# Kernel optimization log

Measured on AMD Instinct MI355X. Metric: run time of the kernel, lower is better.

## Reference

```python
import jax, jax.numpy as jnp
import numpy as np

D_MODEL = 1024
HEADS = 16
D_K = D_MODEL // HEADS


def setup_inputs() -> dict:
    key = jax.random.key(0)
    ks = jax.random.split(key, 9)
    s = 1.0 / np.sqrt(D_MODEL)
    x = jax.random.normal(ks[0], (4, 2048, D_MODEL), dtype=jnp.float32)
    Wq = jax.random.uniform(ks[1], (D_MODEL, D_MODEL), jnp.float32, -s, s)
    Wk = jax.random.uniform(ks[2], (D_MODEL, D_MODEL), jnp.float32, -s, s)
    Wv = jax.random.uniform(ks[3], (D_MODEL, D_MODEL), jnp.float32, -s, s)
    Wo = jax.random.uniform(ks[4], (D_MODEL, D_MODEL), jnp.float32, -s, s)
    bq = jax.random.uniform(ks[5], (D_MODEL,), jnp.float32, -s, s)
    bk = jax.random.uniform(ks[6], (D_MODEL,), jnp.float32, -s, s)
    bv = jax.random.uniform(ks[7], (D_MODEL,), jnp.float32, -s, s)
    bo = jax.random.uniform(ks[8], (D_MODEL,), jnp.float32, -s, s)
    return {"x": x, "Wq": Wq, "bq": bq, "Wk": Wk, "bk": bk,
            "Wv": Wv, "bv": bv, "Wo": Wo, "bo": bo}


def reference(x, Wq, bq, Wk, bk, Wv, bv, Wo, bo):
    B, T, C = x.shape
    H, d_k = HEADS, D_K
    # QKV projections (weights stored as [in, out] -> x @ W + b)
    q = (x @ Wq + bq).reshape(B, T, H, d_k).transpose(0, 2, 1, 3)  # [B,H,T,d_k]
    k = (x @ Wk + bk).reshape(B, T, H, d_k).transpose(0, 2, 1, 3)
    v = (x @ Wv + bv).reshape(B, T, H, d_k).transpose(0, 2, 1, 3)
    scores = jnp.einsum('bhqd,bhkd->bhqk', q, k) / jnp.sqrt(jnp.float32(d_k))
    attn = jax.nn.softmax(scores, axis=-1)
    out = jnp.einsum('bhqk,bhkd->bhqd', attn, v)  # [B,H,T,d_k]
    out = out.transpose(0, 2, 1, 3).reshape(B, T, C)
    return out @ Wo + bo
```

## Files before the change

kernel.cpp:

```cpp
#include <hip/hip_runtime.h>
#include <stdint.h>

typedef _Float16 f16;
typedef _Float16 f16x8 __attribute__((ext_vector_type(8)));
typedef float    f32x4 __attribute__((ext_vector_type(4)));
typedef unsigned int u32x4 __attribute__((ext_vector_type(4)));
typedef unsigned int u32x2 __attribute__((ext_vector_type(2)));
typedef unsigned short u16;

#define MFMA16(A,B,C) __builtin_amdgcn_mfma_f32_16x16x32_f16(A,B,C,0,0,0)

__device__ __forceinline__ void gload_lds16(const void* g, void* l) {
  auto gp = reinterpret_cast<const __attribute__((address_space(1))) unsigned int*>(
      reinterpret_cast<uintptr_t>(g));
  auto lp = reinterpret_cast<__attribute__((address_space(3))) unsigned int*>(
      reinterpret_cast<uintptr_t>(l));
  __builtin_amdgcn_global_load_lds(gp, lp, 16, 0, 0);
}

__device__ __forceinline__ unsigned pk16(float a, float b) {
  unsigned short ua = __builtin_bit_cast(unsigned short, (f16)a);
  unsigned short ub = __builtin_bit_cast(unsigned short, (f16)b);
  return ((unsigned)ub << 16) | (unsigned)ua;
}
__device__ __forceinline__ unsigned pk2rtz(float a, float b) {
  return __builtin_bit_cast(unsigned, __builtin_amdgcn_cvt_pkrtz(a, b));
}
__device__ __forceinline__ float ex2(float x) {
  float r; asm("v_exp_f32 %0, %1" : "=v"(r) : "v"(x)); return r;
}
__device__ __forceinline__ f16x8 asf16(u32x4 v) { return __builtin_bit_cast(f16x8, v); }

#define LOG2E 1.44269504088896f

__global__ __launch_bounds__(256) void k_cvt(const float* __restrict__ in,
                                             u16* __restrict__ out, int n8) {
  int i = blockIdx.x * 256 + threadIdx.x;
  if (i >= n8) return;
  const float4* p = (const float4*)in + (size_t)i * 2;
  float4 a = p[0], b = p[1];
  u32x4 o = { pk16(a.x, a.y), pk16(a.z, a.w), pk16(b.x, b.y), pk16(b.z, b.w) };
  *((u32x4*)out + i) = o;
}

__global__ __launch_bounds__(256) void k_transw(const float* __restrict__ Wq, const float* __restrict__ Wk,
                                                const float* __restrict__ Wv, const float* __restrict__ Wo,
                                                u16* __restrict__ WTq, u16* __restrict__ WTk,
                                                u16* __restrict__ WTv, u16* __restrict__ WTo) {
  int z = blockIdx.z;
  const float* W = (z == 0) ? Wq : (z == 1) ? Wk : (z == 2) ? Wv : Wo;
  u16* WT = (z == 0) ? WTq : (z == 1) ? WTk : (z == 2) ? WTv : WTo;
  __shared__ float tile[64][65];
  int tid = threadIdx.x;
  int r0 = blockIdx.y * 64, c0 = blockIdx.x * 64;
#pragma unroll
  for (int i = 0; i < 4; ++i) {
    int idx = tid + i * 256;
    int row = idx >> 4, ch = (idx & 15) * 4;
    float4 v = *(const float4*)&W[(size_t)(r0 + row) * 1024 + c0 + ch];
    tile[row][ch + 0] = v.x; tile[row][ch + 1] = v.y;
    tile[row][ch + 2] = v.z; tile[row][ch + 3] = v.w;
  }
  __syncthreads();
#pragma unroll
  for (int i = 0; i < 4; ++i) {
    int idx = tid + i * 256;
    int orow = idx >> 4, ch = (idx & 15) * 4;
    u32x2 o = { pk16(tile[ch + 0][orow], tile[ch + 1][orow]),
                pk16(tile[ch + 2][orow], tile[ch + 3][orow]) };
    *(u32x2*)&WT[(size_t)(c0 + orow) * 1024 + r0 + ch] = o;
  }
}

__device__ __forceinline__ void gemm_core(const u16* __restrict__ A, const u16* __restrict__ B,
                                          u16* sA, u16* sB, int m0, int n0, f32x4 acc[4][4]) {
  const int tid = threadIdx.x;
  const int lane = tid & 63;
  const int w = tid >> 6;
  const int wr = w >> 1, wc = w & 1;
  const int c = lane & 15, g = lane >> 4;
#pragma unroll
  for (int i = 0; i < 4; ++i)
#pragma unroll
    for (int j = 0; j < 4; ++j) acc[i][j] = (f32x4){0.f, 0.f, 0.f, 0.f};

  auto stage = [&](int buf, int kt) {
#pragma unroll
    for (int j = 0; j < 2; ++j) {
      int L = j * 4096 + tid * 16;
      int row = L >> 6;
      int chl = (L >> 4) & 3;
      int chg = chl ^ ((row >> 1) & 3);
      gload_lds16(A + (size_t)(m0 + row) * 1024 + kt + chg * 8, (char*)sA + buf * 8192 + L);
      gload_lds16(B + (size_t)(n0 + row) * 1024 + kt + chg * 8, (char*)sB + buf * 8192 + L);
    }
  };

  stage(0, 0);
  stage(1, 32);
  int cur = 0;
  for (int kt = 0; kt < 1024; kt += 32) {
    if (kt < 1024 - 32) {
      asm volatile("s_waitcnt vmcnt(4)" ::: "memory");
    } else {
      asm volatile("s_waitcnt vmcnt(0)" ::: "memory");
    }
    __builtin_amdgcn_s_barrier();
    if (kt + 64 < 1024) {
      int nb = cur + 2; if (nb >= 3) nb -= 3;
      stage(nb, kt + 64);
    }
    const char* cA = (const char*)sA + cur * 8192;
    const char* cB = (const char*)sB + cur * 8192;
    u32x4 av[4], bv[4];
#pragma unroll
    for (int mi = 0; mi < 4; ++mi) {
      int row = wr * 64 + mi * 16 + c;
      av[mi] = *(const u32x4*)(cA + row * 64 + ((g ^ ((row >> 1) & 3)) << 4));
    }
#pragma unroll
    for (int ni = 0; ni < 4; ++ni) {
      int row = wc * 64 + ni * 16 + c;
      bv[ni] = *(const u32x4*)(cB + row * 64 + ((g ^ ((row >> 1) & 3)) << 4));
    }
#pragma unroll
    for (int mi = 0; mi < 4; ++mi)
#pragma unroll
      for (int ni = 0; ni < 4; ++ni)
        acc[mi][ni] = MFMA16(asf16(av[mi]), asf16(bv[ni]), acc[mi][ni]);
    cur = (cur == 2) ? 0 : cur + 1;
  }
}

__global__ __launch_bounds__(256) void k_qkv(const u16* __restrict__ xb,
                                             const u16* __restrict__ wtq, const u16* __restrict__ wtk,
                                             const u16* __restrict__ wtv,
                                             const float* __restrict__ bq, const float* __restrict__ bk,
                                             const float* __restrict__ bv,
                                             u16* __restrict__ Qb, u16* __restrict__ Kb,
                                             u16* __restrict__ VTb) {
  __shared__ alignas(16) u16 sA[3 * 128 * 32];
  __shared__ alignas(16) u16 sB[3 * 128 * 32];
  int m0 = blockIdx.x * 128;
  int nt = blockIdx.y;
  int wsel = nt >> 3;
  int n0 = (nt & 7) * 128;
  const u16* WT = (wsel == 0) ? wtq : (wsel == 1) ? wtk : wtv;
  const float* bias = (wsel == 0) ? bq : (wsel == 1) ? bk : bv;
  f32x4 acc[4][4];
  gemm_core(xb, WT, sA, sB, m0, n0, acc);

  const int lane = threadIdx.x & 63;
  const int w = threadIdx.x >> 6;
  const int wr = w >> 1, wc = w & 1, c = lane & 15, g = lane >> 4;
#pragma unroll
  for (int mi = 0; mi < 4; ++mi) {
#pragma unroll
    for (int ni = 0; ni < 4; ++ni) {
      int ncol = n0 + wc * 64 + ni * 16 + c;
      float bcol = bias[ncol];
      int h = ncol >> 6, d = ncol & 63;
#pragma unroll
      for (int e = 0; e < 4; ++e) {
        int m = m0 + wr * 64 + mi * 16 + g * 4 + e;
        int b = m >> 11, t = m & 2047;
        int bh = (b << 4) | h;
        float val = acc[mi][ni][e] + bcol;
        if (wsel == 0) {
          Qb[((size_t)bh * 2048 + t) * 64 + d] = __builtin_bit_cast(u16, (f16)(val * (0.125f * LOG2E)));
        } else if (wsel == 1) {
          Kb[((size_t)bh * 2048 + t) * 64 + d] = __builtin_bit_cast(u16, (f16)val);
        } else {
          VTb[((size_t)bh * 64 + d) * 2048 + t] = __builtin_bit_cast(u16, (f16)val);
        }
      }
    }
  }
}

__global__ __launch_bounds__(256) void k_attn(const u16* __restrict__ Qb, const u16* __restrict__ Kb,
                                              const u16* __restrict__ VTb, u16* __restrict__ Ob) {
  __shared__ alignas(16) u16 Ks[2][64 * 64];
  __shared__ alignas(16) u16 VTs[2][64 * 64];
  const int tid = threadIdx.x, lane = tid & 63, w = tid >> 6;
  const int c = lane & 15, g = lane >> 4;
  const int lin = blockIdx.x;
  const int bh = (lin & 7) * 8 + (lin >> 7);
  const int qblk = (lin >> 3) & 15;
  const int qw = qblk * 128 + w * 32;
  const size_t kbase = (size_t)bh * 2048 * 64;
  const size_t vbase = (size_t)bh * 64 * 2048;

  u32x4 qa0 = *(const u32x4*)(Qb + ((size_t)bh * 2048 + qw + c) * 64 + g * 8);
  u32x4 qa1 = *(const u32x4*)(Qb + ((size_t)bh * 2048 + qw + c) * 64 + 32 + g * 8);
  u32x4 qa2 = *(const u32x4*)(Qb + ((size_t)bh * 2048 + qw + 16 + c) * 64 + g * 8);
  u32x4 qa3 = *(const u32x4*)(Qb + ((size_t)bh * 2048 + qw + 16 + c) * 64 + 32 + g * 8);

  const u32x4 ONES = { 0x3C003C00u, 0x3C003C00u, 0x3C003C00u, 0x3C003C00u };

  const int L0 = tid * 16, L1 = 4096 + tid * 16;
  const int row0 = L0 >> 7, row1 = L1 >> 7;
  const int chg0 = ((L0 >> 4) & 7) ^ (row0 & 7);
  const int chg1 = ((L1 >> 4) & 7) ^ (row1 & 7);
  const int vchg0 = (chg0 & 4) | ((chg0 & 1) << 1) | ((chg0 >> 1) & 1);
  const int vchg1 = (chg1 & 4) | ((chg1 & 1) << 1) | ((chg1 >> 1) & 1);
  const u16* kg0 = Kb + kbase + (size_t)row0 * 64 + chg0 * 8;
  const u16* kg1 = Kb + kbase + (size_t)row1 * 64 + chg1 * 8;
  const u16* vg0 = VTb + vbase + (size_t)row0 * 2048 + vchg0 * 8;
  const u16* vg1 = VTb + vbase + (size_t)row1 * 2048 + vchg1 * 8;

  auto stage = [&](int buf, int kt) {
    gload_lds16(kg0 + (size_t)kt * 64, (char*)Ks[buf] + L0);
    gload_lds16(kg1 + (size_t)kt * 64, (char*)Ks[buf] + L1);
    gload_lds16(vg0 + kt,              (char*)VTs[buf] + L0);
    gload_lds16(vg1 + kt,              (char*)VTs[buf] + L1);
  };

  const int A0 = c * 128 + ((g ^ (c & 7)) << 4);
  const int A1 = A0 ^ 0x40;

  f32x4 oa[2][4];
  f32x4 la[2];
#pragma unroll
  for (int qb = 0; qb < 2; ++qb) {
    la[qb] = (f32x4){0.f, 0.f, 0.f, 0.f};
#pragma unroll
    for (int i = 0; i < 4; ++i) oa[qb][i] = (f32x4){0.f, 0.f, 0.f, 0.f};
  }

  stage(0, 0);
  __syncthreads();
  int cur = 0;
  for (int kt = 0; kt < 2048; kt += 64) {
    if (kt + 64 < 2048) stage(cur ^ 1, kt + 64);

    unsigned wds[2][8];
    __builtin_amdgcn_s_setprio(1);
    const char* cK = (const char*)Ks[cur];
#pragma unroll
    for (int kb = 0; kb < 4; ++kb) {
      const char* bp = cK + kb * 2048;
      u32x4 k0 = *(const u32x4*)(bp + A0);
      u32x4 k1 = *(const u32x4*)(bp + A1);
      f32x4 z0 = (f32x4){0.f, 0.f, 0.f, 0.f};
      z0 = MFMA16(asf16(k0), asf16(qa0), z0);
      z0 = MFMA16(asf16(k1), asf16(qa1), z0);
      wds[0][kb * 2]     = pk2rtz(ex2(z0[0]), ex2(z0[1]));
      wds[0][kb * 2 + 1] = pk2rtz(ex2(z0[2]), ex2(z0[3]));
      f32x4 z1 = (f32x4){0.f, 0.f, 0.f, 0.f};
      z1 = MFMA16(asf16(k0), asf16(qa2), z1);
      z1 = MFMA16(asf16(k1), asf16(qa3), z1);
      wds[1][kb * 2]     = pk2rtz(ex2(z1[0]), ex2(z1[1]));
      wds[1][kb * 2 + 1] = pk2rtz(ex2(z1[2]), ex2(z1[3]));
    }
    __builtin_amdgcn_s_setprio(0);

    u32x4 pb0[2], pb1[2];
#pragma unroll
    for (int qb = 0; qb < 2; ++qb) {
      unsigned m0 = wds[qb][0], n0 = wds[qb][2];
      unsigned m1 = wds[qb][1], n1 = wds[qb][3];
      unsigned m2 = wds[qb][4], n2 = wds[qb][6];
      unsigned m3 = wds[qb][5], n3 = wds[qb][7];
      asm("v_permlane16_swap_b32 %0, %1" : "+v"(m0), "+v"(n0));
      asm("v_permlane16_swap_b32 %0, %1" : "+v"(m1), "+v"(n1));
      asm("v_permlane16_swap_b32 %0, %1" : "+v"(m2), "+v"(n2));
      asm("v_permlane16_swap_b32 %0, %1" : "+v"(m3), "+v"(n3));
      pb0[qb] = (u32x4){ m0, m1, n0, n1 };
      pb1[qb] = (u32x4){ m2, m3, n2, n3 };
    }

    __builtin_amdgcn_s_setprio(1);
    const char* cV = (const char*)VTs[cur];
#pragma unroll
    for (int db = 0; db < 4; ++db) {
      const char* vp = cV + db * 2048;
      u32x4 v0 = *(const u32x4*)(vp + A0);
      u32x4 v1 = *(const u32x4*)(vp + A1);
      oa[0][db] = MFMA16(asf16(v0), asf16(pb0[0]), oa[0][db]);
      oa[0][db] = MFMA16(asf16(v1), asf16(pb1[0]), oa[0][db]);
      oa[1][db] = MFMA16(asf16(v0), asf16(pb0[1]), oa[1][db]);
      oa[1][db] = MFMA16(asf16(v1), asf16(pb1[1]), oa[1][db]);
    }
    la[0] = MFMA16(asf16(ONES), asf16(pb0[0]), la[0]);
    la[0] = MFMA16(asf16(ONES), asf16(pb1[0]), la[0]);
    la[1] = MFMA16(asf16(ONES), asf16(pb0[1]), la[1]);
    la[1] = MFMA16(asf16(ONES), asf16(pb1[1]), la[1]);
    __builtin_amdgcn_s_setprio(0);

    __syncthreads();
    cur ^= 1;
  }

  int b = bh >> 4, h = bh & 15;
#pragma unroll
  for (int qb = 0; qb < 2; ++qb) {
    float inv = 1.0f / la[qb][0];
    size_t obase = ((size_t)(b * 2048 + qw + qb * 16 + c)) * 1024 + h * 64;
#pragma unroll
    for (int db = 0; db < 4; ++db) {
      int d = db * 16 + g * 4;
      u32x2 o = { pk16(oa[qb][db][0] * inv, oa[qb][db][1] * inv),
                  pk16(oa[qb][db][2] * inv, oa[qb][db][3] * inv) };
      *(u32x2*)(Ob + obase + d) = o;
    }
  }
}

__global__ __launch_bounds__(256) void k_oproj(const u16* __restrict__ Ob, const u16* __restrict__ wto,
                                               const float* __restrict__ bo, float* __restrict__ out) {
  __shared__ alignas(16) u16 sA[3 * 128 * 32];
  __shared__ alignas(16) u16 sB[3 * 128 * 32];
  int m0 = blockIdx.x * 128;
  int n0 = blockIdx.y * 128;
  f32x4 acc[4][4];
  gemm_core(Ob, wto, sA, sB, m0, n0, acc);

  const int lane = threadIdx.x & 63;
  const int w = threadIdx.x >> 6;
  const int wr = w >> 1, wc = w & 1, c = lane & 15, g = lane >> 4;
#pragma unroll
  for (int mi = 0; mi < 4; ++mi) {
#pragma unroll
    for (int ni = 0; ni < 4; ++ni) {
      int ncol = n0 + wc * 64 + ni * 16 + c;
      float bcol = bo[ncol];
#pragma unroll
      for (int e = 0; e < 4; ++e) {
        int m = m0 + wr * 64 + mi * 16 + g * 4 + e;
        out[(size_t)m * 1024 + ncol] = acc[mi][ni][e] + bcol;
      }
    }
  }
}

extern "C" void kernel_launch(void* const* d_in, const int* in_sizes, int n_in,
                              void* d_out, int out_size, void* d_ws, size_t ws_size,
                              hipStream_t stream) {
  const float* x  = (const float*)d_in[0];
  const float* Wq = (const float*)d_in[1];
  const float* bq = (const float*)d_in[2];
  const float* Wk = (const float*)d_in[3];
  const float* bk = (const float*)d_in[4];
  const float* Wv = (const float*)d_in[5];
  const float* bv = (const float*)d_in[6];
  const float* Wo = (const float*)d_in[7];
  const float* bo = (const float*)d_in[8];
  float* out = (float*)d_out;
  char* ws = (char*)d_ws;

  u16* xb  = (u16*)(ws + 0);
  u16* Ob  = (u16*)(ws + 0);
  u16* wtq = (u16*)(ws + 16777216);
  u16* wtk = (u16*)(ws + 18874368);
  u16* wtv = (u16*)(ws + 20971520);
  u16* wto = (u16*)(ws + 23068672);
  u16* Qb  = (u16*)(ws + 25165824);
  u16* Kb  = (u16*)(ws + 41943040);
  u16* VTb = (u16*)(ws + 58720256);

  k_cvt<<<4096, 256, 0, stream>>>(x, xb, 1048576);
  k_transw<<<dim3(16, 16, 4), 256, 0, stream>>>(Wq, Wk, Wv, Wo, wtq, wtk, wtv, wto);
  k_qkv<<<dim3(64, 24), 256, 0, stream>>>(xb, wtq, wtk, wtv, bq, bk, bv, Qb, Kb, VTb);
  k_attn<<<1024, 256, 0, stream>>>(Qb, Kb, VTb, Ob);
  k_oproj<<<dim3(64, 8), 256, 0, stream>>>(Ob, wto, bo, out);
}
```

Before: 197.7 us.

## Fuse prep kernels, switch GEMM to double buffering, swap grid order

```diff
diff --git a/kernel.cpp b/kernel.cpp
--- a/kernel.cpp
+++ b/kernel.cpp
@@ -33,26 +33,26 @@
 
 #define LOG2E 1.44269504088896f
 
-__global__ __launch_bounds__(256) void k_cvt(const float* __restrict__ in,
-                                             u16* __restrict__ out, int n8) {
-  int i = blockIdx.x * 256 + threadIdx.x;
-  if (i >= n8) return;
-  const float4* p = (const float4*)in + (size_t)i * 2;
-  float4 a = p[0], b = p[1];
-  u32x4 o = { pk16(a.x, a.y), pk16(a.z, a.w), pk16(b.x, b.y), pk16(b.z, b.w) };
-  *((u32x4*)out + i) = o;
-}
-
-__global__ __launch_bounds__(256) void k_transw(const float* __restrict__ Wq, const float* __restrict__ Wk,
-                                                const float* __restrict__ Wv, const float* __restrict__ Wo,
-                                                u16* __restrict__ WTq, u16* __restrict__ WTk,
-                                                u16* __restrict__ WTv, u16* __restrict__ WTo) {
-  int z = blockIdx.z;
+__global__ __launch_bounds__(256) void k_prep(const float* __restrict__ x, u16* __restrict__ xb,
+                                              const float* __restrict__ Wq, const float* __restrict__ Wk,
+                                              const float* __restrict__ Wv, const float* __restrict__ Wo,
+                                              u16* __restrict__ WTq, u16* __restrict__ WTk,
+                                              u16* __restrict__ WTv, u16* __restrict__ WTo) {
+  __shared__ float tile[64][65];
+  int tid = threadIdx.x;
+  if (blockIdx.x < 4096) {
+    int i = blockIdx.x * 256 + tid;
+    const float4* p = (const float4*)x + (size_t)i * 2;
+    float4 a = p[0], b = p[1];
+    u32x4 o = { pk16(a.x, a.y), pk16(a.z, a.w), pk16(b.x, b.y), pk16(b.z, b.w) };
+    *((u32x4*)xb + i) = o;
+    return;
+  }
+  int bid = blockIdx.x - 4096;
+  int z = bid >> 8;
   const float* W = (z == 0) ? Wq : (z == 1) ? Wk : (z == 2) ? Wv : Wo;
   u16* WT = (z == 0) ? WTq : (z == 1) ? WTk : (z == 2) ? WTv : WTo;
-  __shared__ float tile[64][65];
-  int tid = threadIdx.x;
-  int r0 = blockIdx.y * 64, c0 = blockIdx.x * 64;
+  int r0 = ((bid >> 4) & 15) * 64, c0 = (bid & 15) * 64;
 #pragma unroll
   for (int i = 0; i < 4; ++i) {
     int idx = tid + i * 256;
@@ -97,19 +97,11 @@
   };
 
   stage(0, 0);
-  stage(1, 32);
   int cur = 0;
   for (int kt = 0; kt < 1024; kt += 32) {
-    if (kt < 1024 - 32) {
-      asm volatile("s_waitcnt vmcnt(4)" ::: "memory");
-    } else {
-      asm volatile("s_waitcnt vmcnt(0)" ::: "memory");
-    }
+    asm volatile("s_waitcnt vmcnt(0)" ::: "memory");
     __builtin_amdgcn_s_barrier();
-    if (kt + 64 < 1024) {
-      int nb = cur + 2; if (nb >= 3) nb -= 3;
-      stage(nb, kt + 64);
-    }
+    if (kt + 32 < 1024) stage(cur ^ 1, kt + 32);
     const char* cA = (const char*)sA + cur * 8192;
     const char* cB = (const char*)sB + cur * 8192;
     u32x4 av[4], bv[4];
@@ -128,21 +120,21 @@
 #pragma unroll
       for (int ni = 0; ni < 4; ++ni)
         acc[mi][ni] = MFMA16(asf16(av[mi]), asf16(bv[ni]), acc[mi][ni]);
-    cur = (cur == 2) ? 0 : cur + 1;
-  }
-}
-
-__global__ __launch_bounds__(256) void k_qkv(const u16* __restrict__ xb,
+    cur ^= 1;
+  }
+}
+
+__global__ __launch_bounds__(256, 5) void k_qkv(const u16* __restrict__ xb,
                                              const u16* __restrict__ wtq, const u16* __restrict__ wtk,
                                              const u16* __restrict__ wtv,
                                              const float* __restrict__ bq, const float* __restrict__ bk,
                                              const float* __restrict__ bv,
                                              u16* __restrict__ Qb, u16* __restrict__ Kb,
                                              u16* __restrict__ VTb) {
-  __shared__ alignas(16) u16 sA[3 * 128 * 32];
-  __shared__ alignas(16) u16 sB[3 * 128 * 32];
-  int m0 = blockIdx.x * 128;
-  int nt = blockIdx.y;
+  __shared__ alignas(16) u16 sA[2 * 128 * 32];
+  __shared__ alignas(16) u16 sB[2 * 128 * 32];
+  int m0 = blockIdx.y * 128;
+  int nt = blockIdx.x;
   int wsel = nt >> 3;
   int n0 = (nt & 7) * 128;
   const u16* WT = (wsel == 0) ? wtq : (wsel == 1) ? wtk : wtv;
@@ -307,12 +299,12 @@
   }
 }
 
-__global__ __launch_bounds__(256) void k_oproj(const u16* __restrict__ Ob, const u16* __restrict__ wto,
+__global__ __launch_bounds__(256, 5) void k_oproj(const u16* __restrict__ Ob, const u16* __restrict__ wto,
                                                const float* __restrict__ bo, float* __restrict__ out) {
-  __shared__ alignas(16) u16 sA[3 * 128 * 32];
-  __shared__ alignas(16) u16 sB[3 * 128 * 32];
-  int m0 = blockIdx.x * 128;
-  int n0 = blockIdx.y * 128;
+  __shared__ alignas(16) u16 sA[2 * 128 * 32];
+  __shared__ alignas(16) u16 sB[2 * 128 * 32];
+  int m0 = blockIdx.y * 128;
+  int n0 = blockIdx.x * 128;
   f32x4 acc[4][4];
   gemm_core(Ob, wto, sA, sB, m0, n0, acc);
 
@@ -359,9 +351,8 @@
   u16* Kb  = (u16*)(ws + 41943040);
   u16* VTb = (u16*)(ws + 58720256);
 
-  k_cvt<<<4096, 256, 0, stream>>>(x, xb, 1048576);
-  k_transw<<<dim3(16, 16, 4), 256, 0, stream>>>(Wq, Wk, Wv, Wo, wtq, wtk, wtv, wto);
-  k_qkv<<<dim3(64, 24), 256, 0, stream>>>(xb, wtq, wtk, wtv, bq, bk, bv, Qb, Kb, VTb);
+  k_prep<<<5120, 256, 0, stream>>>(x, xb, Wq, Wk, Wv, Wo, wtq, wtk, wtv, wto);
+  k_qkv<<<dim3(24, 64), 256, 0, stream>>>(xb, wtq, wtk, wtv, bq, bk, bv, Qb, Kb, VTb);
   k_attn<<<1024, 256, 0, stream>>>(Qb, Kb, VTb, Ob);
-  k_oproj<<<dim3(64, 8), 256, 0, stream>>>(Ob, wto, bo, out);
-}
+  k_oproj<<<dim3(8, 64), 256, 0, stream>>>(Ob, wto, bo, out);
+}
```

Result: slower. 287.2 us (+45.3%).
